# Kernel optimization log

Measured on AMD Instinct MI355X. Metric: run time of the kernel, lower is better.

Reference implementation:

```python
import jax, jax.numpy as jnp
import numpy as np

N, HID, K = 256, 64, 2
B, T_ENC, T_DEC = 64, 12, 12
IN_DIM, OUT_DIM = 2, 1
NUM_SUPPORTS = 2
M = NUM_SUPPORTS * K + 1  # identity + K hops per support


def setup_inputs() -> dict:
    key = jax.random.key(0)
    ks = jax.random.split(key, 16)

    def w(k, shape, scale=0.05):
        return jax.random.normal(k, shape, dtype=jnp.float32) * scale

    def support(k):
        S = jax.random.uniform(k, (N, N), dtype=jnp.float32)
        return S / jnp.sum(S, axis=1, keepdims=True)  # random-walk normalized

    F0e = IN_DIM + HID   # encoder layer-0 concat(input, hidden) feature dim
    F1 = HID + HID       # layer-1 feature dim
    F0d = OUT_DIM + HID  # decoder layer-0 feature dim
    return {
        "encoder_inputs": jax.random.normal(ks[0], (B, T_ENC, N, IN_DIM), dtype=jnp.float32),
        "decoder_inputs": jax.random.normal(ks[1], (B, T_DEC, N, OUT_DIM), dtype=jnp.float32),
        "support0": support(ks[2]),
        "support1": support(ks[3]),
        "enc0_Wg": w(ks[4], (F0e, M, 2 * HID)), "enc0_bg": jnp.ones((2 * HID,), jnp.float32),
        "enc0_Wc": w(ks[5], (F0e, M, HID)),     "enc0_bc": jnp.zeros((HID,), jnp.float32),
        "enc1_Wg": w(ks[6], (F1, M, 2 * HID)),  "enc1_bg": jnp.ones((2 * HID,), jnp.float32),
        "enc1_Wc": w(ks[7], (F1, M, HID)),      "enc1_bc": jnp.zeros((HID,), jnp.float32),
        "dec0_Wg": w(ks[8], (F0d, M, 2 * HID)), "dec0_bg": jnp.ones((2 * HID,), jnp.float32),
        "dec0_Wc": w(ks[9], (F0d, M, HID)),     "dec0_bc": jnp.zeros((HID,), jnp.float32),
        "dec1_Wg": w(ks[10], (F1, M, 2 * HID)), "dec1_bg": jnp.ones((2 * HID,), jnp.float32),
        "dec1_Wc": w(ks[11], (F1, M, HID)),     "dec1_bc": jnp.zeros((HID,), jnp.float32),
        "proj_W": w(ks[12], (HID, OUT_DIM), 0.1),
        "proj_b": jnp.zeros((OUT_DIM,), jnp.float32),
    }


def _diff_conv(supports, x, h, W, b, in_dim):
    # x: (B, N*in_dim), h: (B, N*HID), W: (F, M, O) matching torch flatten order (f*M+m)
    Bsz = x.shape[0]
    xs = jnp.concatenate([x.reshape(Bsz, N, in_dim), h.reshape(Bsz, N, HID)], axis=-1)
    mats = [xs]
    for S in supports:
        x0 = xs
        x1 = jnp.einsum('mn,bnf->bmf', S, xs)
        mats.append(x1)
        for _ in range(2, K + 1):
            x2 = 2.0 * jnp.einsum('mn,bnf->bmf', S, x1) - x0  # Chebyshev recurrence
            mats.append(x2)
            x1, x0 = x2, x1
    X = jnp.stack(mats, axis=2)  # (B, N, M, F)
    out = jnp.einsum('bnmf,fmo->bno', X, W) + b
    return out.reshape(Bsz, -1)


def _cell(supports, x, h, Wg, bg, Wc, bc, in_dim):
    # DCGRUCell: sigmoid gates from diffusion conv, tanh candidate, GRU update
    Bsz = x.shape[0]
    ru = jax.nn.sigmoid(_diff_conv(supports, x, h, Wg, bg, in_dim)).reshape(Bsz, N, 2 * HID)
    r = ru[..., :HID].reshape(Bsz, N * HID)
    u = ru[..., HID:].reshape(Bsz, N * HID)
    c = jnp.tanh(_diff_conv(supports, x, r * h, Wc, bc, in_dim))
    return u * h + (1.0 - u) * c


def _forward(encoder_inputs, decoder_inputs, support0, support1,
             enc0_Wg, enc0_bg, enc0_Wc, enc0_bc, enc1_Wg, enc1_bg, enc1_Wc, enc1_bc,
             dec0_Wg, dec0_bg, dec0_Wc, dec0_bc, dec1_Wg, dec1_bg, dec1_Wc, dec1_bc,
             proj_W, proj_b):
    sup = (support0, support1)
    Bsz = encoder_inputs.shape[0]
    # encoder: (B,T,N,D) -> (T,B,N*D); zero initial hidden
    cur = jnp.transpose(encoder_inputs, (1, 0, 2, 3)).reshape(T_ENC, Bsz, N * IN_DIM)
    enc_params = [(enc0_Wg, enc0_bg, enc0_Wc, enc0_bc, IN_DIM),
                  (enc1_Wg, enc1_bg, enc1_Wc, enc1_bc, HID)]
    h_enc = []
    for (Wg, bg, Wc, bc, ind) in enc_params:
        h0 = jnp.zeros((Bsz, N * HID), cur.dtype)
        def estep(h, x, Wg=Wg, bg=bg, Wc=Wc, bc=bc, ind=ind):
            hn = _cell(sup, x, h, Wg, bg, Wc, bc, ind)
            return hn, hn
        hT, cur = jax.lax.scan(estep, h0, cur)
        h_enc.append(hT)
    # decoder (eval mode: no teacher forcing, dropout off); go symbol = zeros
    dec_params = [(dec0_Wg, dec0_bg, dec0_Wc, dec0_bc, OUT_DIM),
                  (dec1_Wg, dec1_bg, dec1_Wc, dec1_bc, HID)]
    go = jnp.zeros((Bsz, N * OUT_DIM), cur.dtype)

    def dstep(carry, _):
        hs, cur_in = carry
        out = cur_in
        new_hs = []
        for i, (Wg, bg, Wc, bc, ind) in enumerate(dec_params):
            hn = _cell(sup, out, hs[i], Wg, bg, Wc, bc, ind)
            out = hn
            new_hs.append(hn)
        proj = (jnp.einsum('bnh,ho->bno', out.reshape(Bsz, N, HID), proj_W) + proj_b)
        proj = proj.reshape(Bsz, N * OUT_DIM)
        return ((new_hs[0], new_hs[1]), proj), proj

    _, outs = jax.lax.scan(dstep, ((h_enc[0], h_enc[1]), go), None, length=T_DEC)
    outs = outs.reshape(T_DEC, Bsz, N, OUT_DIM)
    return jnp.transpose(outs, (1, 0, 2, 3))  # (B, T_DEC, N, OUT_DIM)


def reference(encoder_inputs, decoder_inputs, support0, support1,
              enc0_Wg, enc0_bg, enc0_Wc, enc0_bc, enc1_Wg, enc1_bg, enc1_Wc, enc1_bc,
              dec0_Wg, dec0_bg, dec0_Wc, dec0_bc, dec1_Wg, dec1_bg, dec1_Wc, dec1_bc,
              proj_W, proj_b):
    return _forward(encoder_inputs, decoder_inputs, support0, support1,
                    enc0_Wg, enc0_bg, enc0_Wc, enc0_bc, enc1_Wg, enc1_bg, enc1_Wc, enc1_bc,
                    dec0_Wg, dec0_bg, dec0_Wc, dec0_bc, dec1_Wg, dec1_bg, dec1_Wc, dec1_bc,
                    proj_W, proj_b)
```

## Files before the change

### kernel.cpp

```cpp
#include <hip/hip_runtime.h>
#include <stdint.h>


typedef short short8 __attribute__((ext_vector_type(8)));
typedef float f32x4 __attribute__((ext_vector_type(4)));
typedef unsigned short ushort4v __attribute__((ext_vector_type(4)));
typedef unsigned long long u64;
typedef u64 u64x2 __attribute__((ext_vector_type(2)));

#define DEVI __device__ __forceinline__

DEVI unsigned short f2bf(float x) {
  unsigned int u = __builtin_bit_cast(unsigned int, x);
  u += 0x7FFFu + ((u >> 16) & 1u);
  return (unsigned short)(u >> 16);
}
DEVI u64 ald(const u64* p) { return __hip_atomic_load(p, __ATOMIC_RELAXED, __HIP_MEMORY_SCOPE_AGENT); }
DEVI void ast(u64* p, u64 v) { __hip_atomic_store(p, v, __ATOMIC_RELAXED, __HIP_MEMORY_SCOPE_AGENT); }
DEVI float aldf(const float* p) { return __hip_atomic_load(p, __ATOMIC_RELAXED, __HIP_MEMORY_SCOPE_AGENT); }
DEVI void astf(float* p, float v) { __hip_atomic_store(p, v, __ATOMIC_RELAXED, __HIP_MEMORY_SCOPE_AGENT); }

struct KP {
  const float* enc_in;
  const float* sup0; const float* sup1;
  const float* Wsrc[8];
  const float* bias[8];
  const float* prW; const float* prB;
  float* out;
  unsigned short* A;
  unsigned short* Wp[8];
  unsigned short* H0[2];
  unsigned short* H1[2];
  unsigned short* RH0;
  unsigned short* RH1;
  float* XD;
  unsigned* ctr;
};

__global__ void prep(KP p) {
  const int i = blockIdx.x, tid = threadIdx.x;
  {
    const int s = i & 1, r = i >> 1;
    const float* S = s ? p.sup1 : p.sup0;
    float acc = 0.f;
    for (int k = 0; k < 256; ++k) acc = fmaf(S[r * 256 + k], S[k * 256 + tid], acc);
    p.A[(2 * s + 0) * 65536 + r * 256 + tid] = f2bf(S[r * 256 + tid]);
    p.A[(2 * s + 1) * 65536 + r * 256 + tid] = f2bf(2.f * acc - (r == tid ? 1.f : 0.f));
  }
  {
    const int gtid = i * 256 + tid;
    const int Fs[8]  = {66, 66, 128, 128, 65, 65, 128, 128};
    const int Os[8]  = {128, 64, 128, 64, 128, 64, 128, 64};
    const int FPs[8] = {96, 96, 128, 128, 96, 96, 128, 128};
    for (int w = 0; w < 8; ++w) {
      const int FPw = FPs[w], KPw = 5 * FPw, tot = Os[w] * KPw;
      for (int e = gtid; e < tot; e += 512 * 256) {
        const int o = e / KPw, k2 = e - o * KPw, m = k2 / FPw, f = k2 - m * FPw;
        p.Wp[w][e] = f2bf((f < Fs[w]) ? p.Wsrc[w][(f * 5 + m) * Os[w] + o] : 0.f);
      }
    }
  }
  {
    const int gtid = i * 256 + tid;
    u64* z0 = (u64*)p.H0[0];
    u64* z1 = (u64*)p.H1[0];
    ast(z0 + 2 * gtid, 0); ast(z0 + 2 * gtid + 1, 0);
    ast(z1 + 2 * gtid, 0); ast(z1 + 2 * gtid + 1, 0);
  }
  if (i == 0 && tid < 64)
    __hip_atomic_store(p.ctr + tid * 64, 0u, __ATOMIC_RELAXED, __HIP_MEMORY_SCOPE_AGENT);
}

template<int IND, int FP, int MODE, bool XSTAGE>
DEVI void dc_stage(int b, int n0, int tid,
                   const float* xf32,
                   const unsigned short* xbf,
                   const unsigned short* hrows,
                   const unsigned short* Amats,
                   const unsigned short* Wp, const float* bias,
                   f32x4 (&hreg)[2], f32x4 (&ureg)[2],
                   unsigned short* grows,
                   const float* projW, const float* projB,
                   float* outp, float* xdout,
                   unsigned short* xsT, unsigned short* Hbuf)
{
  constexpr int O = (MODE == 0) ? 128 : 64;
  constexpr int KPW = 5 * FP;
  constexpr int XS = 264;
  constexpr int HS = 136;
  constexpr int NFT = FP / 16;
  constexpr int NOT_ = O / 16;
  constexpr int FT_W = (NFT + 3) / 4;
  constexpr int OT_W = (NOT_ + 3) / 4;

  const int wv8 = tid >> 6, ln = tid & 63;
  const int l15 = ln & 15, l4 = ln >> 4;
  const int wr = wv8 & 1, wc = wv8 >> 1;
  const int r0 = wr * 32;

  {
    u64 la[4], lb[4];
    const u64* src = (const u64*)hrows;
#pragma unroll
    for (int it = 0; it < 4; ++it) {
      const int g = tid + it * 512;
      la[it] = ald(src + 2 * g); lb[it] = ald(src + 2 * g + 1);
    }
#pragma unroll
    for (int it = 0; it < 4; ++it) {
      const int g = tid + it * 512, row = g >> 5, c = g & 31;
      u64x2 v; v[0] = la[it]; v[1] = lb[it];
      *reinterpret_cast<u64x2*>(&xsT[(IND + row) * XS + c * 8]) = v;
    }
  }
  if (XSTAGE) {
    if (IND == 64) {
      u64 la[4], lb[4];
      const u64* src = (const u64*)xbf;
#pragma unroll
      for (int it = 0; it < 4; ++it) {
        const int g = tid + it * 512;
        la[it] = ald(src + 2 * g); lb[it] = ald(src + 2 * g + 1);
      }
#pragma unroll
      for (int it = 0; it < 4; ++it) {
        const int g = tid + it * 512, row = g >> 5, c = g & 31;
        u64x2 v; v[0] = la[it]; v[1] = lb[it];
        *reinterpret_cast<u64x2*>(&xsT[row * XS + c * 8]) = v;
      }
    } else if (IND == 2) {
      const float v = xf32[tid];
      xsT[(tid & 1) * XS + (tid >> 1)] = f2bf(v);
    } else {
      if (tid < 256) xsT[tid] = xf32 ? f2bf(aldf(xf32 + tid)) : (unsigned short)0;
    }
  }
  __syncthreads();
#pragma unroll
  for (int it = 0; it < FP / 8; ++it) {
    const int e = tid + it * 512, f = e >> 6, nl = e & 63;
    Hbuf[nl * HS + f] = xsT[f * XS + n0 + nl];
  }
  __syncthreads();

  f32x4 pacc[2][OT_W];
#pragma unroll
  for (int rt = 0; rt < 2; ++rt)
#pragma unroll
    for (int oi = 0; oi < OT_W; ++oi) pacc[rt][oi] = 0.f;

  auto proj_step = [&](int m) {
#pragma unroll
    for (int k0 = 0; k0 < FP; k0 += 32) {
      short8 af[2];
#pragma unroll
      for (int rt = 0; rt < 2; ++rt)
        af[rt] = *reinterpret_cast<const short8*>(&Hbuf[(r0 + rt * 16 + l15) * HS + k0 + l4 * 8]);
#pragma unroll
      for (int oi = 0; oi < OT_W; ++oi) {
        const int ot = wc + 4 * oi;
        if (ot < NOT_) {
          short8 bf = *reinterpret_cast<const short8*>(&Wp[(ot * 16 + l15) * KPW + m * FP + k0 + l4 * 8]);
#pragma unroll
          for (int rt = 0; rt < 2; ++rt)
            pacc[rt][oi] = __builtin_amdgcn_mfma_f32_16x16x32_bf16(af[rt], bf, pacc[rt][oi], 0, 0, 0);
        }
      }
    }
  };

  proj_step(0);

  for (int mi = 0; mi < 4; ++mi) {
    const unsigned short* Am = Amats + mi * 65536;
    f32x4 hacc[2][FT_W];
#pragma unroll
    for (int rt = 0; rt < 2; ++rt)
#pragma unroll
      for (int fi = 0; fi < FT_W; ++fi) hacc[rt][fi] = 0.f;

#pragma unroll
    for (int k0 = 0; k0 < 256; k0 += 32) {
      short8 af[2];
#pragma unroll
      for (int rt = 0; rt < 2; ++rt)
        af[rt] = *reinterpret_cast<const short8*>(&Am[(n0 + r0 + rt * 16 + l15) * 256 + k0 + l4 * 8]);
#pragma unroll
      for (int fi = 0; fi < FT_W; ++fi) {
        const int ft = wc + 4 * fi;
        if (ft < NFT) {
          short8 bf = *reinterpret_cast<const short8*>(&xsT[(ft * 16 + l15) * XS + k0 + l4 * 8]);
#pragma unroll
          for (int rt = 0; rt < 2; ++rt)
            hacc[rt][fi] = __builtin_amdgcn_mfma_f32_16x16x32_bf16(af[rt], bf, hacc[rt][fi], 0, 0, 0);
        }
      }
    }
    __syncthreads();
#pragma unroll
    for (int fi = 0; fi < FT_W; ++fi) {
      const int ft = wc + 4 * fi;
      if (ft < NFT) {
#pragma unroll
        for (int rt = 0; rt < 2; ++rt)
#pragma unroll
          for (int j = 0; j < 4; ++j)
            Hbuf[(r0 + rt * 16 + l4 * 4 + j) * HS + ft * 16 + l15] = f2bf(hacc[rt][fi][j]);
      }
    }
    __syncthreads();
    proj_step(mi + 1);
  }

  if (MODE == 0) {
    const float br = bias[wc * 16 + l15];
    const float bu = bias[64 + wc * 16 + l15];
#pragma unroll
    for (int rt = 0; rt < 2; ++rt) {
      f32x4 uu;
      ushort4v pk;
#pragma unroll
      for (int jj = 0; jj < 4; ++jj) {
        const float r = 1.f / (1.f + __expf(-(pacc[rt][0][jj] + br)));
        uu[jj] = 1.f / (1.f + __expf(-(pacc[rt][1][jj] + bu)));
        pk[jj] = f2bf(r * hreg[rt][jj]);
      }
      ureg[rt] = uu;
      ast((u64*)(grows + (wc * 16 + l15) * 256 + n0 + r0 + rt * 16 + l4 * 4),
          __builtin_bit_cast(u64, pk));
    }
  } else {
    float* hrow = reinterpret_cast<float*>(Hbuf);
    if (MODE == 2) __syncthreads();
    const float bc = bias[wc * 16 + l15];
#pragma unroll
    for (int rt = 0; rt < 2; ++rt) {
      f32x4 hn;
      ushort4v pk;
#pragma unroll
      for (int jj = 0; jj < 4; ++jj) {
        const float ex = __expf(2.f * (pacc[rt][0][jj] + bc));
        const float c = 1.f - 2.f / (ex + 1.f);
        hn[jj] = ureg[rt][jj] * hreg[rt][jj] + (1.f - ureg[rt][jj]) * c;
        pk[jj] = f2bf(hn[jj]);
      }
      hreg[rt] = hn;
      ast((u64*)(grows + (wc * 16 + l15) * 256 + n0 + r0 + rt * 16 + l4 * 4),
          __builtin_bit_cast(u64, pk));
      if (MODE == 2) {
#pragma unroll
        for (int jj = 0; jj < 4; ++jj)
          hrow[(r0 + rt * 16 + l4 * 4 + jj) * 68 + wc * 16 + l15] = hn[jj];
      }
    }
    if (MODE == 2) {
      __syncthreads();
      if (tid < 64) {
        float acc = projB[0];
        const float* hr = hrow + tid * 68;
#pragma unroll
        for (int hid = 0; hid < 64; ++hid) acc = fmaf(hr[hid], projW[hid], acc);
        outp[b * 3072 + n0 + tid] = acc;
        astf(xdout + b * 256 + n0 + tid, acc);
      }
    }
  }
}

__launch_bounds__(512, 2)
__global__ void dcrnn_main(KP p) {
  __shared__ __align__(16) unsigned short xsT[128 * 264];
  __shared__ __align__(16) unsigned short Hbuf[64 * 136];
  const int tid = threadIdx.x;
  const int i = (int)blockIdx.x;
  const int q = (i >> 3) & 3;
  const int b = (i & 7) + 8 * (i >> 5);
  const int n0 = q * 64;

  for (int e = tid; e < 128 * 264; e += 512) xsT[e] = 0;
  for (int e = tid; e < 64 * 136; e += 512) Hbuf[e] = 0;
  __syncthreads();

  unsigned* ctr = p.ctr + b * 64;
  unsigned st = 0;
  auto BAR = [&]() {
    ++st;
    asm volatile("s_waitcnt vmcnt(0)" ::: "memory");
    __syncthreads();
    if (tid == 0) {
      __hip_atomic_fetch_add(ctr, 1u, __ATOMIC_RELAXED, __HIP_MEMORY_SCOPE_AGENT);
      const unsigned target = st * 4u;
      while (__hip_atomic_load(ctr, __ATOMIC_RELAXED, __HIP_MEMORY_SCOPE_AGENT) < target)
        __builtin_amdgcn_s_sleep(2);
    }
    __syncthreads();
  };

  f32x4 h0[2], h1[2], u[2];
#pragma unroll
  for (int rt = 0; rt < 2; ++rt) { h0[rt] = 0.f; h1[rt] = 0.f; u[rt] = 0.f; }
  int c0 = 0, c1 = 0;

  for (int t = 0; t < 12; ++t) {
    const float* x0 = p.enc_in + (b * 12 + t) * 512;
    dc_stage<2, 96, 0, true >(b, n0, tid, x0, nullptr, p.H0[c0] + b * 16384, p.A, p.Wp[0], p.bias[0],
                              h0, u, p.RH0 + b * 16384, nullptr, nullptr, nullptr, nullptr, xsT, Hbuf);
    BAR();
    dc_stage<2, 96, 1, false>(b, n0, tid, x0, nullptr, p.RH0 + b * 16384, p.A, p.Wp[1], p.bias[1],
                              h0, u, p.H0[c0 ^ 1] + b * 16384, nullptr, nullptr, nullptr, nullptr, xsT, Hbuf);
    BAR(); c0 ^= 1;
    dc_stage<64, 128, 0, true >(b, n0, tid, nullptr, p.H0[c0] + b * 16384, p.H1[c1] + b * 16384, p.A, p.Wp[2], p.bias[2],
                                h1, u, p.RH1 + b * 16384, nullptr, nullptr, nullptr, nullptr, xsT, Hbuf);
    BAR();
    dc_stage<64, 128, 1, false>(b, n0, tid, nullptr, p.H0[c0] + b * 16384, p.RH1 + b * 16384, p.A, p.Wp[3], p.bias[3],
                                h1, u, p.H1[c1 ^ 1] + b * 16384, nullptr, nullptr, nullptr, nullptr, xsT, Hbuf);
    BAR(); c1 ^= 1;
  }

  for (int t = 0; t < 12; ++t) {
    const float* xd = t ? (p.XD + b * 256) : nullptr;
    dc_stage<1, 96, 0, true >(b, n0, tid, xd, nullptr, p.H0[c0] + b * 16384, p.A, p.Wp[4], p.bias[4],
                              h0, u, p.RH0 + b * 16384, nullptr, nullptr, nullptr, nullptr, xsT, Hbuf);
    BAR();
    dc_stage<1, 96, 1, false>(b, n0, tid, xd, nullptr, p.RH0 + b * 16384, p.A, p.Wp[5], p.bias[5],
                              h0, u, p.H0[c0 ^ 1] + b * 16384, nullptr, nullptr, nullptr, nullptr, xsT, Hbuf);
    BAR(); c0 ^= 1;
    dc_stage<64, 128, 0, true >(b, n0, tid, nullptr, p.H0[c0] + b * 16384, p.H1[c1] + b * 16384, p.A, p.Wp[6], p.bias[6],
                                h1, u, p.RH1 + b * 16384, nullptr, nullptr, nullptr, nullptr, xsT, Hbuf);
    BAR();
    dc_stage<64, 128, 2, false>(b, n0, tid, nullptr, p.H0[c0] + b * 16384, p.RH1 + b * 16384, p.A, p.Wp[7], p.bias[7],
                                h1, u, p.H1[c1 ^ 1] + b * 16384, p.prW, p.prB, p.out + t * 256, p.XD, xsT, Hbuf);
    if (t != 11) BAR();
    c1 ^= 1;
  }
}

extern "C" void kernel_launch(void* const* d_in, const int* in_sizes, int n_in,
                              void* d_out, int out_size, void* d_ws, size_t ws_size,
                              hipStream_t stream)
{
  (void)in_sizes; (void)n_in; (void)out_size; (void)ws_size;
  KP p;
  p.enc_in = (const float*)d_in[0];
  p.sup0 = (const float*)d_in[2];
  p.sup1 = (const float*)d_in[3];
  p.Wsrc[0] = (const float*)d_in[4];  p.bias[0] = (const float*)d_in[5];
  p.Wsrc[1] = (const float*)d_in[6];  p.bias[1] = (const float*)d_in[7];
  p.Wsrc[2] = (const float*)d_in[8];  p.bias[2] = (const float*)d_in[9];
  p.Wsrc[3] = (const float*)d_in[10]; p.bias[3] = (const float*)d_in[11];
  p.Wsrc[4] = (const float*)d_in[12]; p.bias[4] = (const float*)d_in[13];
  p.Wsrc[5] = (const float*)d_in[14]; p.bias[5] = (const float*)d_in[15];
  p.Wsrc[6] = (const float*)d_in[16]; p.bias[6] = (const float*)d_in[17];
  p.Wsrc[7] = (const float*)d_in[18]; p.bias[7] = (const float*)d_in[19];
  p.prW = (const float*)d_in[20];
  p.prB = (const float*)d_in[21];
  p.out = (float*)d_out;

  char* ws = (char*)d_ws;
  size_t off = 0;
  auto carve = [&](size_t bytes) -> char* {
    char* qp = ws + off;
    off += (bytes + 255) & ~(size_t)255;
    return qp;
  };
  p.A = (unsigned short*)carve(4 * 65536 * 2);
  p.Wp[0] = (unsigned short*)carve(128 * 480 * 2);
  p.Wp[1] = (unsigned short*)carve(64 * 480 * 2);
  p.Wp[2] = (unsigned short*)carve(128 * 640 * 2);
  p.Wp[3] = (unsigned short*)carve(64 * 640 * 2);
  p.Wp[4] = (unsigned short*)carve(128 * 480 * 2);
  p.Wp[5] = (unsigned short*)carve(64 * 480 * 2);
  p.Wp[6] = (unsigned short*)carve(128 * 640 * 2);
  p.Wp[7] = (unsigned short*)carve(64 * 640 * 2);
  p.H0[0] = (unsigned short*)carve(64 * 64 * 256 * 2);
  p.H0[1] = (unsigned short*)carve(64 * 64 * 256 * 2);
  p.H1[0] = (unsigned short*)carve(64 * 64 * 256 * 2);
  p.H1[1] = (unsigned short*)carve(64 * 64 * 256 * 2);
  p.RH0 = (unsigned short*)carve(64 * 64 * 256 * 2);
  p.RH1 = (unsigned short*)carve(64 * 64 * 256 * 2);
  p.XD = (float*)carve(64 * 256 * 4);
  p.ctr = (unsigned*)carve(64 * 256);

  prep<<<dim3(512), dim3(256), 0, stream>>>(p);
  dcrnn_main<<<dim3(256), dim3(512), 0, stream>>>(p);
}
```

Before: 2.280 ms.

## Double threads per block so each wave computes one 16-row tile

Raises the block size from 512 to 1024 threads. Each wave now owns a single 16-row strip instead of two, so per-wave MFMA work and accumulator registers are halved and all staging loops are re-strided for 1024 threads. The aim is more waves in flight to hide latency in the latency-bound recurrent stages. The cost is that the A-matrix B-operand fragments are now loaded by twice as many waves, and the launch bound of four 1024-thread blocks per CU may force register spills or be unachievable with the large LDS footprint.

```diff
diff --git a/kernel.cpp b/kernel.cpp
--- a/kernel.cpp
+++ b/kernel.cpp
@@ -78,7 +78,7 @@
                    const unsigned short* hrows,
                    const unsigned short* Amats,
                    const unsigned short* Wp, const float* bias,
-                   f32x4 (&hreg)[2], f32x4 (&ureg)[2],
+                   f32x4& hreg, f32x4& ureg,
                    unsigned short* grows,
                    const float* projW, const float* projB,
                    float* outp, float* xdout,
@@ -93,77 +93,72 @@
   constexpr int FT_W = (NFT + 3) / 4;
   constexpr int OT_W = (NOT_ + 3) / 4;
 
-  const int wv8 = tid >> 6, ln = tid & 63;
+  const int wv = tid >> 6, ln = tid & 63;
   const int l15 = ln & 15, l4 = ln >> 4;
-  const int wr = wv8 & 1, wc = wv8 >> 1;
-  const int r0 = wr * 32;
+  const int wr = wv & 3, wc = wv >> 2;
+  const int r0 = wr * 16;
 
   {
-    u64 la[4], lb[4];
+    u64 la[2], lb[2];
     const u64* src = (const u64*)hrows;
 #pragma unroll
-    for (int it = 0; it < 4; ++it) {
-      const int g = tid + it * 512;
+    for (int it = 0; it < 2; ++it) {
+      const int g = tid + it * 1024;
       la[it] = ald(src + 2 * g); lb[it] = ald(src + 2 * g + 1);
     }
 #pragma unroll
-    for (int it = 0; it < 4; ++it) {
-      const int g = tid + it * 512, row = g >> 5, c = g & 31;
+    for (int it = 0; it < 2; ++it) {
+      const int g = tid + it * 1024, row = g >> 5, c = g & 31;
       u64x2 v; v[0] = la[it]; v[1] = lb[it];
       *reinterpret_cast<u64x2*>(&xsT[(IND + row) * XS + c * 8]) = v;
     }
   }
   if (XSTAGE) {
     if (IND == 64) {
-      u64 la[4], lb[4];
+      u64 la[2], lb[2];
       const u64* src = (const u64*)xbf;
 #pragma unroll
-      for (int it = 0; it < 4; ++it) {
-        const int g = tid + it * 512;
+      for (int it = 0; it < 2; ++it) {
+        const int g = tid + it * 1024;
         la[it] = ald(src + 2 * g); lb[it] = ald(src + 2 * g + 1);
       }
 #pragma unroll
-      for (int it = 0; it < 4; ++it) {
-        const int g = tid + it * 512, row = g >> 5, c = g & 31;
+      for (int it = 0; it < 2; ++it) {
+        const int g = tid + it * 1024, row = g >> 5, c = g & 31;
         u64x2 v; v[0] = la[it]; v[1] = lb[it];
         *reinterpret_cast<u64x2*>(&xsT[row * XS + c * 8]) = v;
       }
     } else if (IND == 2) {
-      const float v = xf32[tid];
-      xsT[(tid & 1) * XS + (tid >> 1)] = f2bf(v);
+      if (tid < 512) {
+        const float v = xf32[tid];
+        xsT[(tid & 1) * XS + (tid >> 1)] = f2bf(v);
+      }
     } else {
       if (tid < 256) xsT[tid] = xf32 ? f2bf(aldf(xf32 + tid)) : (unsigned short)0;
     }
   }
   __syncthreads();
 #pragma unroll
-  for (int it = 0; it < FP / 8; ++it) {
-    const int e = tid + it * 512, f = e >> 6, nl = e & 63;
+  for (int it = 0; it < FP / 16; ++it) {
+    const int e = tid + it * 1024, f = e >> 6, nl = e & 63;
     Hbuf[nl * HS + f] = xsT[f * XS + n0 + nl];
   }
   __syncthreads();
 
-  f32x4 pacc[2][OT_W];
-#pragma unroll
-  for (int rt = 0; rt < 2; ++rt)
-#pragma unroll
-    for (int oi = 0; oi < OT_W; ++oi) pacc[rt][oi] = 0.f;
+  f32x4 pacc[OT_W];
+#pragma unroll
+  for (int oi = 0; oi < OT_W; ++oi) pacc[oi] = 0.f;
 
   auto proj_step = [&](int m) {
 #pragma unroll
     for (int k0 = 0; k0 < FP; k0 += 32) {
-      short8 af[2];
-#pragma unroll
-      for (int rt = 0; rt < 2; ++rt)
-        af[rt] = *reinterpret_cast<const short8*>(&Hbuf[(r0 + rt * 16 + l15) * HS + k0 + l4 * 8]);
+      short8 af = *reinterpret_cast<const short8*>(&Hbuf[(r0 + l15) * HS + k0 + l4 * 8]);
 #pragma unroll
       for (int oi = 0; oi < OT_W; ++oi) {
         const int ot = wc + 4 * oi;
         if (ot < NOT_) {
           short8 bf = *reinterpret_cast<const short8*>(&Wp[(ot * 16 + l15) * KPW + m * FP + k0 + l4 * 8]);
-#pragma unroll
-          for (int rt = 0; rt < 2; ++rt)
-            pacc[rt][oi] = __builtin_amdgcn_mfma_f32_16x16x32_bf16(af[rt], bf, pacc[rt][oi], 0, 0, 0);
+          pacc[oi] = __builtin_amdgcn_mfma_f32_16x16x32_bf16(af, bf, pacc[oi], 0, 0, 0);
         }
       }
     }
@@ -173,26 +168,19 @@
 
   for (int mi = 0; mi < 4; ++mi) {
     const unsigned short* Am = Amats + mi * 65536;
-    f32x4 hacc[2][FT_W];
-#pragma unroll
-    for (int rt = 0; rt < 2; ++rt)
-#pragma unroll
-      for (int fi = 0; fi < FT_W; ++fi) hacc[rt][fi] = 0.f;
+    f32x4 hacc[FT_W];
+#pragma unroll
+    for (int fi = 0; fi < FT_W; ++fi) hacc[fi] = 0.f;
 
 #pragma unroll
     for (int k0 = 0; k0 < 256; k0 += 32) {
-      short8 af[2];
-#pragma unroll
-      for (int rt = 0; rt < 2; ++rt)
-        af[rt] = *reinterpret_cast<const short8*>(&Am[(n0 + r0 + rt * 16 + l15) * 256 + k0 + l4 * 8]);
+      short8 af = *reinterpret_cast<const short8*>(&Am[(n0 + r0 + l15) * 256 + k0 + l4 * 8]);
 #pragma unroll
       for (int fi = 0; fi < FT_W; ++fi) {
         const int ft = wc + 4 * fi;
         if (ft < NFT) {
           short8 bf = *reinterpret_cast<const short8*>(&xsT[(ft * 16 + l15) * XS + k0 + l4 * 8]);
-#pragma unroll
-          for (int rt = 0; rt < 2; ++rt)
-            hacc[rt][fi] = __builtin_amdgcn_mfma_f32_16x16x32_bf16(af[rt], bf, hacc[rt][fi], 0, 0, 0);
+          hacc[fi] = __builtin_amdgcn_mfma_f32_16x16x32_bf16(af, bf, hacc[fi], 0, 0, 0);
         }
       }
     }
@@ -202,10 +190,8 @@
       const int ft = wc + 4 * fi;
       if (ft < NFT) {
 #pragma unroll
-        for (int rt = 0; rt < 2; ++rt)
-#pragma unroll
-          for (int j = 0; j < 4; ++j)
-            Hbuf[(r0 + rt * 16 + l4 * 4 + j) * HS + ft * 16 + l15] = f2bf(hacc[rt][fi][j]);
+        for (int j = 0; j < 4; ++j)
+          Hbuf[(r0 + l4 * 4 + j) * HS + ft * 16 + l15] = f2bf(hacc[fi][j]);
       }
     }
     __syncthreads();
@@ -215,45 +201,37 @@
   if (MODE == 0) {
     const float br = bias[wc * 16 + l15];
     const float bu = bias[64 + wc * 16 + l15];
-#pragma unroll
-    for (int rt = 0; rt < 2; ++rt) {
-      f32x4 uu;
-      ushort4v pk;
-#pragma unroll
-      for (int jj = 0; jj < 4; ++jj) {
-        const float r = 1.f / (1.f + __expf(-(pacc[rt][0][jj] + br)));
-        uu[jj] = 1.f / (1.f + __expf(-(pacc[rt][1][jj] + bu)));
-        pk[jj] = f2bf(r * hreg[rt][jj]);
-      }
-      ureg[rt] = uu;
-      ast((u64*)(grows + (wc * 16 + l15) * 256 + n0 + r0 + rt * 16 + l4 * 4),
-          __builtin_bit_cast(u64, pk));
-    }
+    f32x4 uu;
+    ushort4v pk;
+#pragma unroll
+    for (int jj = 0; jj < 4; ++jj) {
+      const float r = 1.f / (1.f + __expf(-(pacc[0][jj] + br)));
+      uu[jj] = 1.f / (1.f + __expf(-(pacc[1][jj] + bu)));
+      pk[jj] = f2bf(r * hreg[jj]);
+    }
+    ureg = uu;
+    ast((u64*)(grows + (wc * 16 + l15) * 256 + n0 + r0 + l4 * 4),
+        __builtin_bit_cast(u64, pk));
   } else {
     float* hrow = reinterpret_cast<float*>(Hbuf);
     if (MODE == 2) __syncthreads();
     const float bc = bias[wc * 16 + l15];
-#pragma unroll
-    for (int rt = 0; rt < 2; ++rt) {
-      f32x4 hn;
-      ushort4v pk;
-#pragma unroll
-      for (int jj = 0; jj < 4; ++jj) {
-        const float ex = __expf(2.f * (pacc[rt][0][jj] + bc));
-        const float c = 1.f - 2.f / (ex + 1.f);
-        hn[jj] = ureg[rt][jj] * hreg[rt][jj] + (1.f - ureg[rt][jj]) * c;
-        pk[jj] = f2bf(hn[jj]);
-      }
-      hreg[rt] = hn;
-      ast((u64*)(grows + (wc * 16 + l15) * 256 + n0 + r0 + rt * 16 + l4 * 4),
-          __builtin_bit_cast(u64, pk));
-      if (MODE == 2) {
-#pragma unroll
-        for (int jj = 0; jj < 4; ++jj)
-          hrow[(r0 + rt * 16 + l4 * 4 + jj) * 68 + wc * 16 + l15] = hn[jj];
-      }
-    }
+    f32x4 hn;
+    ushort4v pk;
+#pragma unroll
+    for (int jj = 0; jj < 4; ++jj) {
+      const float ex = __expf(2.f * (pacc[0][jj] + bc));
+      const float c = 1.f - 2.f / (ex + 1.f);
+      hn[jj] = ureg[jj] * hreg[jj] + (1.f - ureg[jj]) * c;
+      pk[jj] = f2bf(hn[jj]);
+    }
+    hreg = hn;
+    ast((u64*)(grows + (wc * 16 + l15) * 256 + n0 + r0 + l4 * 4),
+        __builtin_bit_cast(u64, pk));
     if (MODE == 2) {
+#pragma unroll
+      for (int jj = 0; jj < 4; ++jj)
+        hrow[(r0 + l4 * 4 + jj) * 68 + wc * 16 + l15] = hn[jj];
       __syncthreads();
       if (tid < 64) {
         float acc = projB[0];
@@ -267,7 +245,7 @@
   }
 }
 
-__launch_bounds__(512, 2)
+__launch_bounds__(1024, 4)
 __global__ void dcrnn_main(KP p) {
   __shared__ __align__(16) unsigned short xsT[128 * 264];
   __shared__ __align__(16) unsigned short Hbuf[64 * 136];
@@ -277,8 +255,8 @@
   const int b = (i & 7) + 8 * (i >> 5);
   const int n0 = q * 64;
 
-  for (int e = tid; e < 128 * 264; e += 512) xsT[e] = 0;
-  for (int e = tid; e < 64 * 136; e += 512) Hbuf[e] = 0;
+  for (int e = tid; e < 128 * 264; e += 1024) xsT[e] = 0;
+  for (int e = tid; e < 64 * 136; e += 1024) Hbuf[e] = 0;
   __syncthreads();
 
   unsigned* ctr = p.ctr + b * 64;
@@ -296,9 +274,8 @@
     __syncthreads();
   };
 
-  f32x4 h0[2], h1[2], u[2];
-#pragma unroll
-  for (int rt = 0; rt < 2; ++rt) { h0[rt] = 0.f; h1[rt] = 0.f; u[rt] = 0.f; }
+  f32x4 h0, h1, u;
+  h0 = 0.f; h1 = 0.f; u = 0.f;
   int c0 = 0, c1 = 0;
 
   for (int t = 0; t < 12; ++t) {
@@ -382,5 +359,5 @@
   p.ctr = (unsigned*)carve(64 * 256);
 
   prep<<<dim3(512), dim3(256), 0, stream>>>(p);
-  dcrnn_main<<<dim3(256), dim3(512), 0, stream>>>(p);
-}
+  dcrnn_main<<<dim3(256), dim3(1024), 0, stream>>>(p);
+}
```

After: 2.666 ms. +17.0%, slower.

## Fuse gate and candidate stages by recomputing reset gate for all node quarters locally

Applied to the files above, without the earlier changes.

Each cell now runs as one stage per block. Every block recomputes the reset-gate diffusion and projection for all four 64-node quarters of its batch, so it can form r*h for the full graph locally instead of writing it to global memory and waiting at a cross-block barrier. The identity matrix is folded in as a fifth support so all five diffusion terms share one loop, and Hbuf is double-buffered to drop one syncthreads per term. The price is roughly four times the gate diffusion work per block in exchange for half as many inter-block barriers per timestep.

```diff
diff --git a/kernel.cpp b/kernel.cpp
--- a/kernel.cpp
+++ b/kernel.cpp
@@ -14,6 +14,9 @@
   unsigned int u = __builtin_bit_cast(unsigned int, x);
   u += 0x7FFFu + ((u >> 16) & 1u);
   return (unsigned short)(u >> 16);
+}
+DEVI float bf2f(unsigned short s) {
+  return __builtin_bit_cast(float, (unsigned int)s << 16);
 }
 DEVI u64 ald(const u64* p) { return __hip_atomic_load(p, __ATOMIC_RELAXED, __HIP_MEMORY_SCOPE_AGENT); }
 DEVI void ast(u64* p, u64 v) { __hip_atomic_store(p, v, __ATOMIC_RELAXED, __HIP_MEMORY_SCOPE_AGENT); }
@@ -27,12 +30,10 @@
   const float* bias[8];
   const float* prW; const float* prB;
   float* out;
-  unsigned short* A;
+  unsigned short* A5;
   unsigned short* Wp[8];
   unsigned short* H0[2];
   unsigned short* H1[2];
-  unsigned short* RH0;
-  unsigned short* RH1;
   float* XD;
   unsigned* ctr;
 };
@@ -44,8 +45,9 @@
     const float* S = s ? p.sup1 : p.sup0;
     float acc = 0.f;
     for (int k = 0; k < 256; ++k) acc = fmaf(S[r * 256 + k], S[k * 256 + tid], acc);
-    p.A[(2 * s + 0) * 65536 + r * 256 + tid] = f2bf(S[r * 256 + tid]);
-    p.A[(2 * s + 1) * 65536 + r * 256 + tid] = f2bf(2.f * acc - (r == tid ? 1.f : 0.f));
+    if (s == 0) p.A5[r * 256 + tid] = (r == tid) ? (unsigned short)0x3F80 : (unsigned short)0;
+    p.A5[(1 + 2 * s) * 65536 + r * 256 + tid] = f2bf(S[r * 256 + tid]);
+    p.A5[(2 + 2 * s) * 65536 + r * 256 + tid] = f2bf(2.f * acc - (r == tid ? 1.f : 0.f));
   }
   {
     const int gtid = i * 256 + tid;
@@ -71,31 +73,29 @@
     __hip_atomic_store(p.ctr + tid * 64, 0u, __ATOMIC_RELAXED, __HIP_MEMORY_SCOPE_AGENT);
 }
 
-template<int IND, int FP, int MODE, bool XSTAGE>
-DEVI void dc_stage(int b, int n0, int tid,
-                   const float* xf32,
-                   const unsigned short* xbf,
-                   const unsigned short* hrows,
-                   const unsigned short* Amats,
-                   const unsigned short* Wp, const float* bias,
-                   f32x4 (&hreg)[2], f32x4 (&ureg)[2],
-                   unsigned short* grows,
-                   const float* projW, const float* projB,
-                   float* outp, float* xdout,
-                   unsigned short* xsT, unsigned short* Hbuf)
+template<int IND, int FP, int MODE>
+DEVI void cell_stage(int b, int q, int n0, int tid,
+                     const float* xf32,
+                     const unsigned short* xbf,
+                     const unsigned short* hrows,
+                     const unsigned short* A5,
+                     const unsigned short* Wg, const float* bg,
+                     const unsigned short* Wc, const float* bc,
+                     f32x4 (&hreg)[2],
+                     unsigned short* hout,
+                     const float* projW, const float* projB,
+                     float* outp, float* xdout,
+                     unsigned short* xsT, unsigned short* Hbuf)
 {
-  constexpr int O = (MODE == 0) ? 128 : 64;
   constexpr int KPW = 5 * FP;
   constexpr int XS = 264;
   constexpr int HS = 136;
+  constexpr int HB = 64 * HS;
   constexpr int NFT = FP / 16;
-  constexpr int NOT_ = O / 16;
-  constexpr int FT_W = (NFT + 3) / 4;
-  constexpr int OT_W = (NOT_ + 3) / 4;
-
-  const int wv8 = tid >> 6, ln = tid & 63;
+
+  const int wv = tid >> 6, ln = tid & 63;
   const int l15 = ln & 15, l4 = ln >> 4;
-  const int wr = wv8 & 1, wc = wv8 >> 1;
+  const int wr = wv & 1, wc = wv >> 1;
   const int r0 = wr * 32;
 
   {
@@ -112,73 +112,125 @@
       u64x2 v; v[0] = la[it]; v[1] = lb[it];
       *reinterpret_cast<u64x2*>(&xsT[(IND + row) * XS + c * 8]) = v;
     }
-  }
-  if (XSTAGE) {
     if (IND == 64) {
-      u64 la[4], lb[4];
-      const u64* src = (const u64*)xbf;
+      u64 xa[4], xb2[4];
+      const u64* src2 = (const u64*)xbf;
 #pragma unroll
       for (int it = 0; it < 4; ++it) {
         const int g = tid + it * 512;
-        la[it] = ald(src + 2 * g); lb[it] = ald(src + 2 * g + 1);
+        xa[it] = ald(src2 + 2 * g); xb2[it] = ald(src2 + 2 * g + 1);
       }
 #pragma unroll
       for (int it = 0; it < 4; ++it) {
         const int g = tid + it * 512, row = g >> 5, c = g & 31;
-        u64x2 v; v[0] = la[it]; v[1] = lb[it];
+        u64x2 v; v[0] = xa[it]; v[1] = xb2[it];
         *reinterpret_cast<u64x2*>(&xsT[row * XS + c * 8]) = v;
       }
     } else if (IND == 2) {
-      const float v = xf32[tid];
-      xsT[(tid & 1) * XS + (tid >> 1)] = f2bf(v);
+      xsT[(tid & 1) * XS + (tid >> 1)] = f2bf(xf32[tid]);
     } else {
       if (tid < 256) xsT[tid] = xf32 ? f2bf(aldf(xf32 + tid)) : (unsigned short)0;
     }
   }
   __syncthreads();
-#pragma unroll
-  for (int it = 0; it < FP / 8; ++it) {
-    const int e = tid + it * 512, f = e >> 6, nl = e & 63;
-    Hbuf[nl * HS + f] = xsT[f * XS + n0 + nl];
-  }
+
+  f32x4 pr[4][2], pu[2];
+#pragma unroll
+  for (int rq = 0; rq < 4; ++rq)
+#pragma unroll
+    for (int rt = 0; rt < 2; ++rt) pr[rq][rt] = 0.f;
+#pragma unroll
+  for (int rt = 0; rt < 2; ++rt) pu[rt] = 0.f;
+
+#pragma unroll
+  for (int rq = 0; rq < 4; ++rq) {
+    for (int m = 0; m < 5; ++m) {
+      const unsigned short* Am = A5 + m * 65536;
+      f32x4 hacc[2][2];
+#pragma unroll
+      for (int rt = 0; rt < 2; ++rt) { hacc[rt][0] = 0.f; hacc[rt][1] = 0.f; }
+#pragma unroll
+      for (int k0 = 0; k0 < 256; k0 += 32) {
+        short8 af[2];
+#pragma unroll
+        for (int rt = 0; rt < 2; ++rt)
+          af[rt] = *reinterpret_cast<const short8*>(&Am[(rq * 64 + r0 + rt * 16 + l15) * 256 + k0 + l4 * 8]);
+#pragma unroll
+        for (int fi = 0; fi < 2; ++fi) {
+          const int ft = wc + 4 * fi;
+          if (ft < NFT) {
+            short8 bf = *reinterpret_cast<const short8*>(&xsT[(ft * 16 + l15) * XS + k0 + l4 * 8]);
+#pragma unroll
+            for (int rt = 0; rt < 2; ++rt)
+              hacc[rt][fi] = __builtin_amdgcn_mfma_f32_16x16x32_bf16(af[rt], bf, hacc[rt][fi], 0, 0, 0);
+          }
+        }
+      }
+      unsigned short* dst = Hbuf + ((rq * 5 + m) & 1) * HB;
+#pragma unroll
+      for (int fi = 0; fi < 2; ++fi) {
+        const int ft = wc + 4 * fi;
+        if (ft < NFT) {
+#pragma unroll
+          for (int rt = 0; rt < 2; ++rt)
+#pragma unroll
+            for (int j = 0; j < 4; ++j)
+              dst[(r0 + rt * 16 + l4 * 4 + j) * HS + ft * 16 + l15] = f2bf(hacc[rt][fi][j]);
+        }
+      }
+      __syncthreads();
+#pragma unroll
+      for (int k0 = 0; k0 < FP; k0 += 32) {
+        short8 af2[2];
+#pragma unroll
+        for (int rt = 0; rt < 2; ++rt)
+          af2[rt] = *reinterpret_cast<const short8*>(&dst[(r0 + rt * 16 + l15) * HS + k0 + l4 * 8]);
+        short8 bfr = *reinterpret_cast<const short8*>(&Wg[(wc * 16 + l15) * KPW + m * FP + k0 + l4 * 8]);
+#pragma unroll
+        for (int rt = 0; rt < 2; ++rt)
+          pr[rq][rt] = __builtin_amdgcn_mfma_f32_16x16x32_bf16(af2[rt], bfr, pr[rq][rt], 0, 0, 0);
+        if (rq == q) {
+          short8 bfu = *reinterpret_cast<const short8*>(&Wg[((4 + wc) * 16 + l15) * KPW + m * FP + k0 + l4 * 8]);
+#pragma unroll
+          for (int rt = 0; rt < 2; ++rt)
+            pu[rt] = __builtin_amdgcn_mfma_f32_16x16x32_bf16(af2[rt], bfu, pu[rt], 0, 0, 0);
+        }
+      }
+    }
+  }
+
+  const float br = bg[wc * 16 + l15];
+  const float bu = bg[64 + wc * 16 + l15];
+  f32x4 u[2];
+#pragma unroll
+  for (int rt = 0; rt < 2; ++rt)
+#pragma unroll
+    for (int jj = 0; jj < 4; ++jj)
+      u[rt][jj] = 1.f / (1.f + __expf(-(pu[rt][jj] + bu)));
+#pragma unroll
+  for (int rq = 0; rq < 4; ++rq)
+#pragma unroll
+    for (int rt = 0; rt < 2; ++rt) {
+      unsigned short* ap = &xsT[(IND + wc * 16 + l15) * XS + rq * 64 + r0 + rt * 16 + l4 * 4];
+      ushort4v hv = *reinterpret_cast<ushort4v*>(ap);
+      ushort4v pk;
+#pragma unroll
+      for (int jj = 0; jj < 4; ++jj) {
+        const float r = 1.f / (1.f + __expf(-(pr[rq][rt][jj] + br)));
+        pk[jj] = f2bf(r * bf2f(hv[jj]));
+      }
+      *reinterpret_cast<ushort4v*>(ap) = pk;
+    }
   __syncthreads();
 
-  f32x4 pacc[2][OT_W];
-#pragma unroll
-  for (int rt = 0; rt < 2; ++rt)
-#pragma unroll
-    for (int oi = 0; oi < OT_W; ++oi) pacc[rt][oi] = 0.f;
-
-  auto proj_step = [&](int m) {
-#pragma unroll
-    for (int k0 = 0; k0 < FP; k0 += 32) {
-      short8 af[2];
-#pragma unroll
-      for (int rt = 0; rt < 2; ++rt)
-        af[rt] = *reinterpret_cast<const short8*>(&Hbuf[(r0 + rt * 16 + l15) * HS + k0 + l4 * 8]);
-#pragma unroll
-      for (int oi = 0; oi < OT_W; ++oi) {
-        const int ot = wc + 4 * oi;
-        if (ot < NOT_) {
-          short8 bf = *reinterpret_cast<const short8*>(&Wp[(ot * 16 + l15) * KPW + m * FP + k0 + l4 * 8]);
-#pragma unroll
-          for (int rt = 0; rt < 2; ++rt)
-            pacc[rt][oi] = __builtin_amdgcn_mfma_f32_16x16x32_bf16(af[rt], bf, pacc[rt][oi], 0, 0, 0);
-        }
-      }
-    }
-  };
-
-  proj_step(0);
-
-  for (int mi = 0; mi < 4; ++mi) {
-    const unsigned short* Am = Amats + mi * 65536;
-    f32x4 hacc[2][FT_W];
-#pragma unroll
-    for (int rt = 0; rt < 2; ++rt)
-#pragma unroll
-      for (int fi = 0; fi < FT_W; ++fi) hacc[rt][fi] = 0.f;
-
+  f32x4 pc[2];
+#pragma unroll
+  for (int rt = 0; rt < 2; ++rt) pc[rt] = 0.f;
+  for (int m = 0; m < 5; ++m) {
+    const unsigned short* Am = A5 + m * 65536;
+    f32x4 hacc[2][2];
+#pragma unroll
+    for (int rt = 0; rt < 2; ++rt) { hacc[rt][0] = 0.f; hacc[rt][1] = 0.f; }
 #pragma unroll
     for (int k0 = 0; k0 < 256; k0 += 32) {
       short8 af[2];
@@ -186,7 +238,7 @@
       for (int rt = 0; rt < 2; ++rt)
         af[rt] = *reinterpret_cast<const short8*>(&Am[(n0 + r0 + rt * 16 + l15) * 256 + k0 + l4 * 8]);
 #pragma unroll
-      for (int fi = 0; fi < FT_W; ++fi) {
+      for (int fi = 0; fi < 2; ++fi) {
         const int ft = wc + 4 * fi;
         if (ft < NFT) {
           short8 bf = *reinterpret_cast<const short8*>(&xsT[(ft * 16 + l15) * XS + k0 + l4 * 8]);
@@ -196,73 +248,63 @@
         }
       }
     }
-    __syncthreads();
-#pragma unroll
-    for (int fi = 0; fi < FT_W; ++fi) {
+    unsigned short* dst = Hbuf + (m & 1) * HB;
+#pragma unroll
+    for (int fi = 0; fi < 2; ++fi) {
       const int ft = wc + 4 * fi;
       if (ft < NFT) {
 #pragma unroll
         for (int rt = 0; rt < 2; ++rt)
 #pragma unroll
           for (int j = 0; j < 4; ++j)
-            Hbuf[(r0 + rt * 16 + l4 * 4 + j) * HS + ft * 16 + l15] = f2bf(hacc[rt][fi][j]);
+            dst[(r0 + rt * 16 + l4 * 4 + j) * HS + ft * 16 + l15] = f2bf(hacc[rt][fi][j]);
       }
     }
     __syncthreads();
-    proj_step(mi + 1);
-  }
-
-  if (MODE == 0) {
-    const float br = bias[wc * 16 + l15];
-    const float bu = bias[64 + wc * 16 + l15];
-#pragma unroll
-    for (int rt = 0; rt < 2; ++rt) {
-      f32x4 uu;
-      ushort4v pk;
-#pragma unroll
-      for (int jj = 0; jj < 4; ++jj) {
-        const float r = 1.f / (1.f + __expf(-(pacc[rt][0][jj] + br)));
-        uu[jj] = 1.f / (1.f + __expf(-(pacc[rt][1][jj] + bu)));
-        pk[jj] = f2bf(r * hreg[rt][jj]);
-      }
-      ureg[rt] = uu;
-      ast((u64*)(grows + (wc * 16 + l15) * 256 + n0 + r0 + rt * 16 + l4 * 4),
-          __builtin_bit_cast(u64, pk));
-    }
-  } else {
-    float* hrow = reinterpret_cast<float*>(Hbuf);
-    if (MODE == 2) __syncthreads();
-    const float bc = bias[wc * 16 + l15];
-#pragma unroll
-    for (int rt = 0; rt < 2; ++rt) {
-      f32x4 hn;
-      ushort4v pk;
-#pragma unroll
-      for (int jj = 0; jj < 4; ++jj) {
-        const float ex = __expf(2.f * (pacc[rt][0][jj] + bc));
-        const float c = 1.f - 2.f / (ex + 1.f);
-        hn[jj] = ureg[rt][jj] * hreg[rt][jj] + (1.f - ureg[rt][jj]) * c;
-        pk[jj] = f2bf(hn[jj]);
-      }
-      hreg[rt] = hn;
-      ast((u64*)(grows + (wc * 16 + l15) * 256 + n0 + r0 + rt * 16 + l4 * 4),
-          __builtin_bit_cast(u64, pk));
-      if (MODE == 2) {
-#pragma unroll
-        for (int jj = 0; jj < 4; ++jj)
-          hrow[(r0 + rt * 16 + l4 * 4 + jj) * 68 + wc * 16 + l15] = hn[jj];
-      }
-    }
+#pragma unroll
+    for (int k0 = 0; k0 < FP; k0 += 32) {
+      short8 af2[2];
+#pragma unroll
+      for (int rt = 0; rt < 2; ++rt)
+        af2[rt] = *reinterpret_cast<const short8*>(&dst[(r0 + rt * 16 + l15) * HS + k0 + l4 * 8]);
+      short8 bfc = *reinterpret_cast<const short8*>(&Wc[(wc * 16 + l15) * KPW + m * FP + k0 + l4 * 8]);
+#pragma unroll
+      for (int rt = 0; rt < 2; ++rt)
+        pc[rt] = __builtin_amdgcn_mfma_f32_16x16x32_bf16(af2[rt], bfc, pc[rt], 0, 0, 0);
+    }
+  }
+
+  const float bcb = bc[wc * 16 + l15];
+  float* hrow = reinterpret_cast<float*>(Hbuf + HB);
+#pragma unroll
+  for (int rt = 0; rt < 2; ++rt) {
+    f32x4 hn;
+    ushort4v pk;
+#pragma unroll
+    for (int jj = 0; jj < 4; ++jj) {
+      const float ex = __expf(2.f * (pc[rt][jj] + bcb));
+      const float c = 1.f - 2.f / (ex + 1.f);
+      hn[jj] = u[rt][jj] * hreg[rt][jj] + (1.f - u[rt][jj]) * c;
+      pk[jj] = f2bf(hn[jj]);
+    }
+    hreg[rt] = hn;
+    ast((u64*)(hout + (wc * 16 + l15) * 256 + n0 + r0 + rt * 16 + l4 * 4),
+        __builtin_bit_cast(u64, pk));
     if (MODE == 2) {
-      __syncthreads();
-      if (tid < 64) {
-        float acc = projB[0];
-        const float* hr = hrow + tid * 68;
-#pragma unroll
-        for (int hid = 0; hid < 64; ++hid) acc = fmaf(hr[hid], projW[hid], acc);
-        outp[b * 3072 + n0 + tid] = acc;
-        astf(xdout + b * 256 + n0 + tid, acc);
-      }
+#pragma unroll
+      for (int jj = 0; jj < 4; ++jj)
+        hrow[(r0 + rt * 16 + l4 * 4 + jj) * 68 + wc * 16 + l15] = hn[jj];
+    }
+  }
+  if (MODE == 2) {
+    __syncthreads();
+    if (tid < 64) {
+      float acc = projB[0];
+      const float* hr = hrow + tid * 68;
+#pragma unroll
+      for (int hid = 0; hid < 64; ++hid) acc = fmaf(hr[hid], projW[hid], acc);
+      outp[b * 3072 + n0 + tid] = acc;
+      astf(xdout + b * 256 + n0 + tid, acc);
     }
   }
 }
@@ -270,7 +312,7 @@
 __launch_bounds__(512, 2)
 __global__ void dcrnn_main(KP p) {
   __shared__ __align__(16) unsigned short xsT[128 * 264];
-  __shared__ __align__(16) unsigned short Hbuf[64 * 136];
+  __shared__ __align__(16) unsigned short Hbuf[2 * 64 * 136];
   const int tid = threadIdx.x;
   const int i = (int)blockIdx.x;
   const int q = (i >> 3) & 3;
@@ -278,7 +320,7 @@
   const int n0 = q * 64;
 
   for (int e = tid; e < 128 * 264; e += 512) xsT[e] = 0;
-  for (int e = tid; e < 64 * 136; e += 512) Hbuf[e] = 0;
+  for (int e = tid; e < 2 * 64 * 136; e += 512) Hbuf[e] = 0;
   __syncthreads();
 
   unsigned* ctr = p.ctr + b * 64;
@@ -296,40 +338,32 @@
     __syncthreads();
   };
 
-  f32x4 h0[2], h1[2], u[2];
-#pragma unroll
-  for (int rt = 0; rt < 2; ++rt) { h0[rt] = 0.f; h1[rt] = 0.f; u[rt] = 0.f; }
+  f32x4 h0[2], h1[2];
+#pragma unroll
+  for (int rt = 0; rt < 2; ++rt) { h0[rt] = 0.f; h1[rt] = 0.f; }
   int c0 = 0, c1 = 0;
 
   for (int t = 0; t < 12; ++t) {
     const float* x0 = p.enc_in + (b * 12 + t) * 512;
-    dc_stage<2, 96, 0, true >(b, n0, tid, x0, nullptr, p.H0[c0] + b * 16384, p.A, p.Wp[0], p.bias[0],
-                              h0, u, p.RH0 + b * 16384, nullptr, nullptr, nullptr, nullptr, xsT, Hbuf);
-    BAR();
-    dc_stage<2, 96, 1, false>(b, n0, tid, x0, nullptr, p.RH0 + b * 16384, p.A, p.Wp[1], p.bias[1],
-                              h0, u, p.H0[c0 ^ 1] + b * 16384, nullptr, nullptr, nullptr, nullptr, xsT, Hbuf);
+    cell_stage<2, 96, 1>(b, q, n0, tid, x0, nullptr, p.H0[c0] + b * 16384, p.A5,
+                         p.Wp[0], p.bias[0], p.Wp[1], p.bias[1], h0,
+                         p.H0[c0 ^ 1] + b * 16384, nullptr, nullptr, nullptr, nullptr, xsT, Hbuf);
     BAR(); c0 ^= 1;
-    dc_stage<64, 128, 0, true >(b, n0, tid, nullptr, p.H0[c0] + b * 16384, p.H1[c1] + b * 16384, p.A, p.Wp[2], p.bias[2],
-                                h1, u, p.RH1 + b * 16384, nullptr, nullptr, nullptr, nullptr, xsT, Hbuf);
-    BAR();
-    dc_stage<64, 128, 1, false>(b, n0, tid, nullptr, p.H0[c0] + b * 16384, p.RH1 + b * 16384, p.A, p.Wp[3], p.bias[3],
-                                h1, u, p.H1[c1 ^ 1] + b * 16384, nullptr, nullptr, nullptr, nullptr, xsT, Hbuf);
+    cell_stage<64, 128, 1>(b, q, n0, tid, nullptr, p.H0[c0] + b * 16384, p.H1[c1] + b * 16384, p.A5,
+                           p.Wp[2], p.bias[2], p.Wp[3], p.bias[3], h1,
+                           p.H1[c1 ^ 1] + b * 16384, nullptr, nullptr, nullptr, nullptr, xsT, Hbuf);
     BAR(); c1 ^= 1;
   }
 
   for (int t = 0; t < 12; ++t) {
     const float* xd = t ? (p.XD + b * 256) : nullptr;
-    dc_stage<1, 96, 0, true >(b, n0, tid, xd, nullptr, p.H0[c0] + b * 16384, p.A, p.Wp[4], p.bias[4],
-                              h0, u, p.RH0 + b * 16384, nullptr, nullptr, nullptr, nullptr, xsT, Hbuf);
-    BAR();
-    dc_stage<1, 96, 1, false>(b, n0, tid, xd, nullptr, p.RH0 + b * 16384, p.A, p.Wp[5], p.bias[5],
-                              h0, u, p.H0[c0 ^ 1] + b * 16384, nullptr, nullptr, nullptr, nullptr, xsT, Hbuf);
+    cell_stage<1, 96, 1>(b, q, n0, tid, xd, nullptr, p.H0[c0] + b * 16384, p.A5,
+                         p.Wp[4], p.bias[4], p.Wp[5], p.bias[5], h0,
+                         p.H0[c0 ^ 1] + b * 16384, nullptr, nullptr, nullptr, nullptr, xsT, Hbuf);
     BAR(); c0 ^= 1;
-    dc_stage<64, 128, 0, true >(b, n0, tid, nullptr, p.H0[c0] + b * 16384, p.H1[c1] + b * 16384, p.A, p.Wp[6], p.bias[6],
-                                h1, u, p.RH1 + b * 16384, nullptr, nullptr, nullptr, nullptr, xsT, Hbuf);
-    BAR();
-    dc_stage<64, 128, 2, false>(b, n0, tid, nullptr, p.H0[c0] + b * 16384, p.RH1 + b * 16384, p.A, p.Wp[7], p.bias[7],
-                                h1, u, p.H1[c1 ^ 1] + b * 16384, p.prW, p.prB, p.out + t * 256, p.XD, xsT, Hbuf);
+    cell_stage<64, 128, 2>(b, q, n0, tid, nullptr, p.H0[c0] + b * 16384, p.H1[c1] + b * 16384, p.A5,
+                           p.Wp[6], p.bias[6], p.Wp[7], p.bias[7], h1,
+                           p.H1[c1 ^ 1] + b * 16384, p.prW, p.prB, p.out + t * 256, p.XD, xsT, Hbuf);
     if (t != 11) BAR();
     c1 ^= 1;
   }
@@ -363,7 +397,7 @@
     off += (bytes + 255) & ~(size_t)255;
     return qp;
   };
-  p.A = (unsigned short*)carve(4 * 65536 * 2);
+  p.A5 = (unsigned short*)carve(5 * 65536 * 2);
   p.Wp[0] = (unsigned short*)carve(128 * 480 * 2);
   p.Wp[1] = (unsigned short*)carve(64 * 480 * 2);
   p.Wp[2] = (unsigned short*)carve(128 * 640 * 2);
@@ -376,8 +410,6 @@
   p.H0[1] = (unsigned short*)carve(64 * 64 * 256 * 2);
   p.H1[0] = (unsigned short*)carve(64 * 64 * 256 * 2);
   p.H1[1] = (unsigned short*)carve(64 * 64 * 256 * 2);
-  p.RH0 = (unsigned short*)carve(64 * 64 * 256 * 2);
-  p.RH1 = (unsigned short*)carve(64 * 64 * 256 * 2);
   p.XD = (float*)carve(64 * 256 * 4);
   p.ctr = (unsigned*)carve(64 * 256);
 
```

Result: slower. 5.754 ms (+152.4%).
